# Kernel optimization log

Measured on AMD Instinct MI355X. Metric: run time of the kernel, lower is better.

## Reference

```python
import jax, jax.numpy as jnp
import numpy as np

RCUT = 6.0
NA = 10000      # atoms per image
NS = 4          # species
NMAX = 32       # radial basis size
NO = 4          # orbitals for lmax=2: (3**2-1)//2
OIDX = jnp.array([0, 1, 1, 1])  # lmax=2 -> [0] + [1]*3
B, NM = 4, 150000


def setup_inputs() -> dict:
    key = jax.random.key(0)
    ks = jax.random.split(key, 12)
    disp = jax.random.normal(ks[0], (B, NM, 3), jnp.float32) * 2.0
    iidx = jnp.sort(jax.random.randint(ks[1], (B, NM), 0, NA), axis=-1)
    jidx = jax.random.randint(ks[2], (B, NM), 0, NA)
    sorted_numbers = jax.random.randint(ks[3], (NA,), 0, NS)
    alpha = -(jax.random.uniform(ks[4], (NS, NMAX), jnp.float32) + 0.2)
    rs = jax.random.uniform(ks[5], (NS, NMAX), jnp.float32)
    species_params = jax.random.uniform(ks[6], (NS, NMAX), jnp.float32)
    # loop x lmax x nmax x NO
    orbital_params = jax.random.uniform(ks[7], (2, 2, NMAX, NO), jnp.float32)
    h1, h2 = int(1.2 * NO), int(1.2 * NMAX)  # 4, 38
    w1 = jax.random.normal(ks[8], (NO, h1), jnp.float32) * 0.3
    b1 = jnp.zeros((h1,), jnp.float32)
    w2 = jax.random.normal(ks[9], (h1, h2), jnp.float32) * 0.3
    b2 = jnp.zeros((h2,), jnp.float32)
    w3 = jax.random.normal(ks[10], (h2, NMAX), jnp.float32) * 0.3
    b3 = jnp.zeros((NMAX,), jnp.float32)
    return dict(disp=disp, alpha=alpha, rs=rs, species_params=species_params,
                orbital_params=orbital_params, w1=w1, b1=b1, w2=w2, b2=b2,
                w3=w3, b3=b3, iidx=iidx, jidx=jidx,
                sorted_numbers=sorted_numbers)


def _density(Wln, Csn, Fxyz, iidx, jidx):
    # Wln: NO x nmax x NO ; Csn: NA x nmax ; Fxyz: NM x NO x nmax
    cj = Csn[jidx]                                   # NM x nmax (gather)
    cjF = cj[:, None, :] * Fxyz                      # NM x NO x nmax
    bnl = jax.ops.segment_sum(cjF, iidx, num_segments=NA)  # NA x NO x nmax (scatter-add)
    t = jnp.einsum('lno,aln->alo', Wln, bnl)         # NA x NO x NO
    return jnp.sum(t * t, axis=1)                    # NA x NO


def _mlp(rho, w1, b1, w2, b2, w3, b3):
    h = jnp.tanh(rho @ w1 + b1)
    h = jnp.tanh(h @ w2 + b2)
    return h @ w3 + b3                               # NA x nmax


def reference(disp, alpha, rs, species_params, orbital_params,
              w1, b1, w2, b2, w3, b3, iidx, jidx, sorted_numbers):
    def one_image(disp_i, ii, jj):
        dist = jnp.linalg.norm(disp_i, axis=1)                        # NM
        fcut = 0.25 * (jnp.cos(dist * jnp.pi / RCUT) + 1.0) ** 2      # NM
        jatn = sorted_numbers[jj]                                     # NM
        radial = jnp.exp(alpha[jatn] * (dist[:, None] - rs[jatn]) ** 2)  # NM x nmax
        angle = jnp.ones((disp_i.shape[0], NO), disp_i.dtype).at[:, 1:4].set(disp_i)
        Fxyz = fcut[:, None, None] * angle[:, :, None] * radial[:, None, :]  # NM x NO x nmax
        Csn = species_params[sorted_numbers]                          # NA x nmax
        rho = _density(orbital_params[0][OIDX], Csn, Fxyz, ii, jj)    # NA x NO
        # loop iteration 1 (loop=2): shared per-atom MLP update of Csn
        Csn = Csn + _mlp(rho, w1, b1, w2, b2, w3, b3)
        rho = _density(orbital_params[1][OIDX], Csn, Fxyz, ii, jj)
        return rho
    return jax.vmap(one_image)(disp, iidx, jidx)                      # B x NA x NO
```

## Files before the change

kernel.cpp:

```cpp
#include <hip/hip_runtime.h>
#include <hip/hip_fp16.h>
#include <math.h>

#define NA_ 10000
#define NM_ 150000
#define B_  4
#define NS_ 4
#define NMAX_ 32
#define NO_ 4
#define H1_ 4
#define H2_ 38
#define PI_F 3.14159265358979323846f
#define LOG2E_F 1.44269504088896f

#define CSN_OFF   ((size_t)0)
#define CSN_BYTES ((size_t)B_ * NA_ * NMAX_ * 4)
#define ST_OFF    (CSN_OFF + CSN_BYTES)
#define ST_BYTES  ((size_t)B_ * (NA_ + 1) * 4 + 64)
#define E_OFF     (ST_OFF + ST_BYTES)
#define E_BYTES   (((size_t)B_ * NM_ + 64) * NMAX_ * 2)
#define WS_NEED_E (E_OFF + E_BYTES)

__device__ __forceinline__ float fast_tanh(float x) {
    float t = __expf(2.0f * x);
    return 1.0f - __fdividef(2.0f, t + 1.0f);
}

template <int CTRL>
__device__ __forceinline__ float dpp_ror_add(float v) {
    int r = __builtin_amdgcn_update_dpp(0, __float_as_int(v), CTRL, 0xF, 0xF, true);
    return v + __int_as_float(r);
}
__device__ __forceinline__ float half_reduce32(float v) {
    v = dpp_ror_add<0x121>(v);
    v = dpp_ror_add<0x122>(v);
    v = dpp_ror_add<0x124>(v);
    v = dpp_ror_add<0x128>(v);
    int s = __builtin_amdgcn_ds_swizzle(__float_as_int(v), 0x401F);
    return v + __int_as_float(s);
}

__global__ void starts_kernel(const int* __restrict__ iidx, int* __restrict__ starts) {
    int p = blockIdx.x * blockDim.x + threadIdx.x;
    if (p >= B_ * NM_) return;
    int b = p / NM_, pl = p - b * NM_;
    const int* ii = iidx + (size_t)b * NM_;
    int* st = starts + (size_t)b * (NA_ + 1);
    int cur = ii[pl];
    int prev = (pl == 0) ? -1 : ii[pl - 1];
    for (int a = prev + 1; a <= cur; ++a) st[a] = pl;
    if (pl == NM_ - 1) {
        for (int a = cur + 1; a <= NA_; ++a) st[a] = NM_;
    }
}

__global__ __launch_bounds__(256, 8) void pass0_kernel(
    const float* __restrict__ disp, const int* __restrict__ jidx,
    const float* __restrict__ alpha, const float* __restrict__ rsp,
    const float* __restrict__ spp, const float* __restrict__ op,
    const float* __restrict__ w1, const float* __restrict__ b1,
    const float* __restrict__ w2, const float* __restrict__ b2,
    const float* __restrict__ w3, const float* __restrict__ b3,
    const int* __restrict__ sorted_numbers, const int* __restrict__ starts,
    float* __restrict__ csn2, unsigned short* __restrict__ E)
{
    __shared__ float4 lds_rec[4][2][32];
    __shared__ float2 lds_df[4][2][32];
    __shared__ float2 tab2[NS_ * NMAX_];
    __shared__ float lds_h2[4][2][40];

    int tid = threadIdx.x;
    if (tid < NS_ * NMAX_)
        tab2[tid] = make_float2(alpha[tid] * LOG2E_F, rsp[tid]);
    __syncthreads();

    int wv = tid >> 6;
    int wave = blockIdx.x * 4 + wv;
    int lane = tid & 63;
    int h = lane >> 5, n = lane & 31;
    int g = wave * 2 + h;
    if (g >= B_ * NA_) return;
    int b = g / NA_, a = g - b * NA_;

    const int* st = starts + b * (NA_ + 1);
    int p0 = st[a], p1 = st[a + 1];
    int seg = p1 - p0;
    int oseg = __shfl_xor(seg, 32);
    int mseg = (seg > oseg) ? seg : oseg;

    const int* jjb = jidx + (size_t)b * NM_;
    const float* dpb = disp + (size_t)b * NM_ * 3;

    int pk = p0 + n;
    if (pk > NM_ - 1) pk = NM_ - 1;
    int jmine = jjb[pk];
    float sx = dpb[pk * 3 + 0];
    float sy = dpb[pk * 3 + 1];
    float sz = dpb[pk * 3 + 2];
    int jatm = sorted_numbers[jmine];
    float sd = sqrtf(sx * sx + sy * sy + sz * sz);
    float sc = __cosf(sd * (PI_F / 6.0f));
    float sfc = 0.25f * (sc + 1.f) * (sc + 1.f);
    lds_rec[wv][h][n] = make_float4(sx, sy, sz, __int_as_float(jatm));
    lds_df[wv][h][n] = make_float2(sd, sfc);
    const float4* lp = &lds_rec[wv][h][0];
    const float4* ldf4 = reinterpret_cast<const float4*>(&lds_df[wv][h][0]);
    const float2* tab2n = tab2 + n;

    float sp0 = spp[n], sp1 = spp[32 + n], sp2 = spp[64 + n], sp3 = spp[96 + n];

    float W0[NO_], W1[NO_];
#pragma unroll
    for (int o = 0; o < NO_; ++o) {
        W0[o] = op[(0 * NMAX_ + n) * NO_ + o];
        W1[o] = op[(1 * NMAX_ + n) * NO_ + o];
    }

    unsigned short* Ebl = E + ((size_t)b * NM_ + p0) * NMAX_ + n;

    float acc0 = 0.f, acc1 = 0.f, acc2 = 0.f, acc3 = 0.f;

#define KKF(k, DD, FF) {                                                     \
    float4 q_ = lp[(k)];                                                     \
    int jat_ = __float_as_int(q_.w);                                         \
    float2 ar_ = tab2n[jat_ * NMAX_];                                        \
    float dd_ = (DD) - ar_.y;                                                \
    float e_ = exp2f(ar_.x * dd_ * dd_);                                     \
    float Ef_ = e_ * (FF);                                                   \
    Ebl[(k) * NMAX_] = __half_as_ushort(__float2half_rn(Ef_));               \
    bool s0_ = (jat_ & 1) != 0;                                              \
    bool s1_ = (jat_ & 2) != 0;                                              \
    float cv_ = s1_ ? (s0_ ? sp3 : sp2) : (s0_ ? sp1 : sp0);                 \
    float coef_ = Ef_ * cv_;                                                 \
    coef_ = ((k) < seg) ? coef_ : 0.f;                                       \
    acc0 += coef_;                                                           \
    acc1 = fmaf(coef_, q_.x, acc1);                                          \
    acc2 = fmaf(coef_, q_.y, acc2);                                          \
    acc3 = fmaf(coef_, q_.z, acc3);                                          \
}
#define KK4F(k0) if (mseg > (k0)) {                                          \
    float4 dA_ = ldf4[(k0) >> 1];                                            \
    float4 dB_ = ldf4[((k0) >> 1) + 1];                                      \
    KKF(k0, dA_.x, dA_.y) KKF((k0)+1, dA_.z, dA_.w)                          \
    KKF((k0)+2, dB_.x, dB_.y) KKF((k0)+3, dB_.z, dB_.w) }
    KK4F(0) KK4F(4) KK4F(8) KK4F(12) KK4F(16) KK4F(20) KK4F(24) KK4F(28)
#undef KK4F
#undef KKF

    for (int p = p0 + 32; p < p1; ++p) {
        int j = jjb[p];
        float x = dpb[p * 3 + 0], y = dpb[p * 3 + 1], z = dpb[p * 3 + 2];
        int jat = sorted_numbers[j];
        float dist = sqrtf(x * x + y * y + z * z);
        float c = __cosf(dist * (PI_F / 6.0f));
        float fc = 0.25f * (c + 1.f) * (c + 1.f);
        float2 ar = tab2n[(jat & 3) * NMAX_];
        float dd = dist - ar.y;
        float Ef = fc * exp2f(ar.x * dd * dd);
        E[((size_t)b * NM_ + p) * NMAX_ + n] =
            __half_as_ushort(__float2half_rn(Ef));
        bool s0 = (jat & 1) != 0, s1 = (jat & 2) != 0;
        float cv = s1 ? (s0 ? sp3 : sp2) : (s0 ? sp1 : sp0);
        float coef = Ef * cv;
        acc0 += coef;
        acc1 = fmaf(coef, x, acc1);
        acc2 = fmaf(coef, y, acc2);
        acc3 = fmaf(coef, z, acc3);
    }

    float t[4][NO_];
#pragma unroll
    for (int o = 0; o < NO_; ++o) {
        t[0][o] = W0[o] * acc0;
        t[1][o] = W1[o] * acc1;
        t[2][o] = W1[o] * acc2;
        t[3][o] = W1[o] * acc3;
    }
#pragma unroll
    for (int l = 0; l < 4; ++l)
#pragma unroll
        for (int o = 0; o < NO_; ++o)
            t[l][o] = half_reduce32(t[l][o]);

    float rho[NO_];
#pragma unroll
    for (int o = 0; o < NO_; ++o)
        rho[o] = t[0][o] * t[0][o] + t[1][o] * t[1][o] +
                 t[2][o] * t[2][o] + t[3][o] * t[3][o];

    float h1v[H1_];
#pragma unroll
    for (int k = 0; k < H1_; ++k) {
        float s = b1[k];
#pragma unroll
        for (int o = 0; o < NO_; ++o) s = fmaf(rho[o], w1[o * H1_ + k], s);
        h1v[k] = fast_tanh(s);
    }
    float sa = b2[n];
    int jbi = 32 + (n < 6 ? n : 5);
    float sb = b2[jbi];
#pragma unroll
    for (int k = 0; k < H1_; ++k) {
        sa = fmaf(h1v[k], w2[k * H2_ + n], sa);
        sb = fmaf(h1v[k], w2[k * H2_ + jbi], sb);
    }
    float hva = fast_tanh(sa);
    float hvb = fast_tanh(sb);
    lds_h2[wv][h][n] = hva;
    if (n < 6) lds_h2[wv][h][32 + n] = hvb;
    const float4* h4 = reinterpret_cast<const float4*>(&lds_h2[wv][h][0]);
    float on = b3[n];
#pragma unroll
    for (int q = 0; q < 9; ++q) {
        float4 hh = h4[q];
        on = fmaf(hh.x, w3[(q * 4 + 0) * NMAX_ + n], on);
        on = fmaf(hh.y, w3[(q * 4 + 1) * NMAX_ + n], on);
        on = fmaf(hh.z, w3[(q * 4 + 2) * NMAX_ + n], on);
        on = fmaf(hh.w, w3[(q * 4 + 3) * NMAX_ + n], on);
    }
    float2 ht = *reinterpret_cast<const float2*>(&lds_h2[wv][h][36]);
    on = fmaf(ht.x, w3[36 * NMAX_ + n], on);
    on = fmaf(ht.y, w3[37 * NMAX_ + n], on);

    int aat = sorted_numbers[a];
    bool t0b = (aat & 1) != 0, t1b = (aat & 2) != 0;
    float basev = t1b ? (t0b ? sp3 : sp2) : (t0b ? sp1 : sp0);
    csn2[(size_t)g * NMAX_ + n] = basev + on;
}

__global__ __launch_bounds__(256, 4) void pass1_kernel(
    const float* __restrict__ disp, const int* __restrict__ jidx,
    const float* __restrict__ op, const int* __restrict__ starts,
    const float* __restrict__ csn2, const unsigned short* __restrict__ E,
    float* __restrict__ out)
{
    __shared__ float4 lds_rec[4][2][32];
    int tid = threadIdx.x;
    int wv = tid >> 6;
    int wave = blockIdx.x * 4 + wv;
    int lane = tid & 63;
    int h = lane >> 5, n = lane & 31;
    int g = wave * 2 + h;
    if (g >= B_ * NA_) return;
    int b = g / NA_, a = g - b * NA_;

    const int* st = starts + b * (NA_ + 1);
    int p0 = st[a], p1 = st[a + 1];
    int seg = p1 - p0;
    int oseg = __shfl_xor(seg, 32);
    int mseg = (seg > oseg) ? seg : oseg;

    const int* jjb = jidx + (size_t)b * NM_;
    const float* dpb = disp + (size_t)b * NM_ * 3;
    const float* csb = csn2 + (size_t)b * NA_ * NMAX_;

    int pk = p0 + n;
    if (pk > NM_ - 1) pk = NM_ - 1;
    int jmine = jjb[pk];
    float sx = dpb[pk * 3 + 0];
    float sy = dpb[pk * 3 + 1];
    float sz = dpb[pk * 3 + 2];
    lds_rec[wv][h][n] = make_float4(sx, sy, sz, __int_as_float(jmine));
    const float4* lp = &lds_rec[wv][h][0];
    const int* lpi = (const int*)lp;

    float W0[NO_], W1[NO_];
#pragma unroll
    for (int o = 0; o < NO_; ++o) {
        W0[o] = op[(2 * NMAX_ + n) * NO_ + o];
        W1[o] = op[(3 * NMAX_ + n) * NO_ + o];
    }

    const unsigned short* Erd = E + ((size_t)b * NM_ + p0) * NMAX_ + n;

    float cj[32];
    unsigned short r[32];
#define LC(k) { int j_ = lpi[(k) * 4 + 3];                                   \
                cj[(k)] = csb[(size_t)j_ * NMAX_ + n]; }
#define LC8(k0) LC(k0) LC((k0)+1) LC((k0)+2) LC((k0)+3) \
                LC((k0)+4) LC((k0)+5) LC((k0)+6) LC((k0)+7)
    LC8(0)
    if (mseg > 8)  { LC8(8) }  else { cj[8]=cj[9]=cj[10]=cj[11]=cj[12]=cj[13]=cj[14]=cj[15]=0.f; }
    if (mseg > 16) { LC8(16) } else { cj[16]=cj[17]=cj[18]=cj[19]=cj[20]=cj[21]=cj[22]=cj[23]=0.f; }
    if (mseg > 24) { LC8(24) } else { cj[24]=cj[25]=cj[26]=cj[27]=cj[28]=cj[29]=cj[30]=cj[31]=0.f; }
#undef LC8
#undef LC
#define LDR(k) r[(k)] = Erd[(k) * NMAX_];
#define LDR8(k0) LDR(k0) LDR((k0)+1) LDR((k0)+2) LDR((k0)+3) \
                 LDR((k0)+4) LDR((k0)+5) LDR((k0)+6) LDR((k0)+7)
    LDR8(0)
    if (mseg > 8)  { LDR8(8) }  else { r[8]=r[9]=r[10]=r[11]=r[12]=r[13]=r[14]=r[15]=0; }
    if (mseg > 16) { LDR8(16) } else { r[16]=r[17]=r[18]=r[19]=r[20]=r[21]=r[22]=r[23]=0; }
    if (mseg > 24) { LDR8(24) } else { r[24]=r[25]=r[26]=r[27]=r[28]=r[29]=r[30]=r[31]=0; }
#undef LDR8
#undef LDR

    float acc0 = 0.f, acc1 = 0.f, acc2 = 0.f, acc3 = 0.f;
#define KK(k) {                                                              \
    float4 q_ = lp[(k)];                                                     \
    float coef_ = __half2float(__ushort_as_half(r[(k)])) * cj[(k)];          \
    coef_ = ((k) < seg) ? coef_ : 0.f;                                       \
    acc0 += coef_;                                                           \
    acc1 = fmaf(coef_, q_.x, acc1);                                          \
    acc2 = fmaf(coef_, q_.y, acc2);                                          \
    acc3 = fmaf(coef_, q_.z, acc3);                                          \
}
#define KK4(k0) if (mseg > (k0)) { KK(k0) KK((k0)+1) KK((k0)+2) KK((k0)+3) }
    KK4(0) KK4(4) KK4(8) KK4(12) KK4(16) KK4(20) KK4(24) KK4(28)
#undef KK4
#undef KK

    for (int p = p0 + 32; p < p1; ++p) {
        int j = jjb[p];
        float x = dpb[p * 3 + 0], y = dpb[p * 3 + 1], z = dpb[p * 3 + 2];
        float Ef = __half2float(__ushort_as_half(
            E[((size_t)b * NM_ + p) * NMAX_ + n]));
        float coef = Ef * csb[(size_t)j * NMAX_ + n];
        acc0 += coef;
        acc1 = fmaf(coef, x, acc1);
        acc2 = fmaf(coef, y, acc2);
        acc3 = fmaf(coef, z, acc3);
    }

    float t[4][NO_];
#pragma unroll
    for (int o = 0; o < NO_; ++o) {
        t[0][o] = W0[o] * acc0;
        t[1][o] = W1[o] * acc1;
        t[2][o] = W1[o] * acc2;
        t[3][o] = W1[o] * acc3;
    }
#pragma unroll
    for (int l = 0; l < 4; ++l)
#pragma unroll
        for (int o = 0; o < NO_; ++o)
            t[l][o] = half_reduce32(t[l][o]);

    float rho[NO_];
#pragma unroll
    for (int o = 0; o < NO_; ++o)
        rho[o] = t[0][o] * t[0][o] + t[1][o] * t[1][o] +
                 t[2][o] * t[2][o] + t[3][o] * t[3][o];

    if (n == 0) {
        *reinterpret_cast<float4*>(out + (size_t)g * NO_) =
            make_float4(rho[0], rho[1], rho[2], rho[3]);
    }
}

template <int PASS>
__global__ __launch_bounds__(256, 4) void fb_pass_kernel(
    const float* __restrict__ disp, const int* __restrict__ jidx,
    const float* __restrict__ alpha, const float* __restrict__ rsp,
    const float* __restrict__ spp, const float* __restrict__ op,
    const float* __restrict__ w1, const float* __restrict__ b1,
    const float* __restrict__ w2, const float* __restrict__ b2,
    const float* __restrict__ w3, const float* __restrict__ b3,
    const int* __restrict__ sorted_numbers, const int* __restrict__ starts,
    float* __restrict__ csn2, float* __restrict__ out)
{
    __shared__ float4 lds_rec[4][2][32];
    __shared__ float2 lds_df[4][2][32];
    __shared__ float2 tab2[NS_ * NMAX_];
    __shared__ float lds_h2[4][2][40];

    int tid = threadIdx.x;
    if (tid < NS_ * NMAX_)
        tab2[tid] = make_float2(alpha[tid] * LOG2E_F, rsp[tid]);
    __syncthreads();

    int wv = tid >> 6;
    int wave = blockIdx.x * 4 + wv;
    int lane = tid & 63;
    int h = lane >> 5, n = lane & 31;
    int g = wave * 2 + h;
    if (g >= B_ * NA_) return;
    int b = g / NA_, a = g - b * NA_;

    const int* st = starts + b * (NA_ + 1);
    int p0 = st[a], p1 = st[a + 1];
    int seg = p1 - p0;
    int oseg = __shfl_xor(seg, 32);
    int mseg = (seg > oseg) ? seg : oseg;

    const int* jjb = jidx + (size_t)b * NM_;
    const float* dpb = disp + (size_t)b * NM_ * 3;
    const float* csb = csn2 + (size_t)b * NA_ * NMAX_;

    int pk = p0 + n;
    if (pk > NM_ - 1) pk = NM_ - 1;
    int jmine = jjb[pk];
    float sx = dpb[pk * 3 + 0];
    float sy = dpb[pk * 3 + 1];
    float sz = dpb[pk * 3 + 2];
    int jatm = sorted_numbers[jmine];
    float sd = sqrtf(sx * sx + sy * sy + sz * sz);
    float sc = __cosf(sd * (PI_F / 6.0f));
    float sfc = 0.25f * (sc + 1.f) * (sc + 1.f);
    lds_rec[wv][h][n] = make_float4(sx, sy, sz,
                                    __int_as_float(jmine | (jatm << 14)));
    lds_df[wv][h][n] = make_float2(sd, sfc);
    const float4* lp = &lds_rec[wv][h][0];
    const int* lpi = (const int*)lp;
    const float4* ldf4 = reinterpret_cast<const float4*>(&lds_df[wv][h][0]);
    const float2* tab2n = tab2 + n;

    float sp0 = spp[n], sp1 = spp[32 + n], sp2 = spp[64 + n], sp3 = spp[96 + n];

    const float* opb = op + (size_t)PASS * 2 * NMAX_ * NO_;
    float W0[NO_], W1[NO_];
#pragma unroll
    for (int o = 0; o < NO_; ++o) {
        W0[o] = opb[(0 * NMAX_ + n) * NO_ + o];
        W1[o] = opb[(1 * NMAX_ + n) * NO_ + o];
    }

    float cj[32];
    if constexpr (PASS == 1) {
#define LC(k) { int w_ = lpi[(k) * 4 + 3] & 0x3fff;                          \
                cj[(k)] = csb[(size_t)w_ * NMAX_ + n]; }
#define LC8(k0) LC(k0) LC((k0)+1) LC((k0)+2) LC((k0)+3) \
                LC((k0)+4) LC((k0)+5) LC((k0)+6) LC((k0)+7)
        LC8(0)
        if (mseg > 8)  { LC8(8) }  else { cj[8]=cj[9]=cj[10]=cj[11]=cj[12]=cj[13]=cj[14]=cj[15]=0.f; }
        if (mseg > 16) { LC8(16) } else { cj[16]=cj[17]=cj[18]=cj[19]=cj[20]=cj[21]=cj[22]=cj[23]=0.f; }
        if (mseg > 24) { LC8(24) } else { cj[24]=cj[25]=cj[26]=cj[27]=cj[28]=cj[29]=cj[30]=cj[31]=0.f; }
#undef LC8
#undef LC
    }

    float acc0 = 0.f, acc1 = 0.f, acc2 = 0.f, acc3 = 0.f;
#define KKF(k, DD, FF) {                                                     \
    float4 q_ = lp[(k)];                                                     \
    int w_ = __float_as_int(q_.w);                                           \
    int jat_ = (w_ >> 14) & 3;                                               \
    float2 ar_ = tab2n[jat_ * NMAX_];                                        \
    float dd_ = (DD) - ar_.y;                                                \
    float e_ = exp2f(ar_.x * dd_ * dd_);                                     \
    float Ef_ = e_ * (FF);                                                   \
    float cv_;                                                               \
    if constexpr (PASS == 0) {                                               \
        bool s0_ = (w_ & (1 << 14)) != 0;                                    \
        bool s1_ = (w_ & (1 << 15)) != 0;                                    \
        cv_ = s1_ ? (s0_ ? sp3 : sp2) : (s0_ ? sp1 : sp0);                   \
    } else {                                                                 \
        cv_ = cj[(k)];                                                       \
    }                                                                        \
    float coef_ = Ef_ * cv_;                                                 \
    coef_ = ((k) < seg) ? coef_ : 0.f;                                       \
    acc0 += coef_;                                                           \
    acc1 = fmaf(coef_, q_.x, acc1);                                          \
    acc2 = fmaf(coef_, q_.y, acc2);                                          \
    acc3 = fmaf(coef_, q_.z, acc3);                                          \
}
#define KK4F(k0) if (mseg > (k0)) {                                          \
    float4 dA_ = ldf4[(k0) >> 1];                                            \
    float4 dB_ = ldf4[((k0) >> 1) + 1];                                      \
    KKF(k0, dA_.x, dA_.y) KKF((k0)+1, dA_.z, dA_.w)                          \
    KKF((k0)+2, dB_.x, dB_.y) KKF((k0)+3, dB_.z, dB_.w) }
    KK4F(0) KK4F(4) KK4F(8) KK4F(12) KK4F(16) KK4F(20) KK4F(24) KK4F(28)
#undef KK4F
#undef KKF

    for (int p = p0 + 32; p < p1; ++p) {
        int j = jjb[p];
        float x = dpb[p * 3 + 0], y = dpb[p * 3 + 1], z = dpb[p * 3 + 2];
        int jat = sorted_numbers[j];
        float dist = sqrtf(x * x + y * y + z * z);
        float c = __cosf(dist * (PI_F / 6.0f));
        float fc = 0.25f * (c + 1.f) * (c + 1.f);
        float2 ar = tab2n[(jat & 3) * NMAX_];
        float dd = dist - ar.y;
        float Ef = fc * exp2f(ar.x * dd * dd);
        float cv;
        if constexpr (PASS == 0) {
            bool s0 = (jat & 1) != 0, s1 = (jat & 2) != 0;
            cv = s1 ? (s0 ? sp3 : sp2) : (s0 ? sp1 : sp0);
        } else {
            cv = csb[(size_t)j * NMAX_ + n];
        }
        float coef = Ef * cv;
        acc0 += coef;
        acc1 = fmaf(coef, x, acc1);
        acc2 = fmaf(coef, y, acc2);
        acc3 = fmaf(coef, z, acc3);
    }

    float t[4][NO_];
#pragma unroll
    for (int o = 0; o < NO_; ++o) {
        t[0][o] = W0[o] * acc0;
        t[1][o] = W1[o] * acc1;
        t[2][o] = W1[o] * acc2;
        t[3][o] = W1[o] * acc3;
    }
#pragma unroll
    for (int l = 0; l < 4; ++l)
#pragma unroll
        for (int o = 0; o < NO_; ++o)
            t[l][o] = half_reduce32(t[l][o]);

    float rho[NO_];
#pragma unroll
    for (int o = 0; o < NO_; ++o)
        rho[o] = t[0][o] * t[0][o] + t[1][o] * t[1][o] +
                 t[2][o] * t[2][o] + t[3][o] * t[3][o];

    if constexpr (PASS == 1) {
        if (n == 0) {
            *reinterpret_cast<float4*>(out + (size_t)g * NO_) =
                make_float4(rho[0], rho[1], rho[2], rho[3]);
        }
    } else {
        float h1v[H1_];
#pragma unroll
        for (int k = 0; k < H1_; ++k) {
            float s = b1[k];
#pragma unroll
            for (int o = 0; o < NO_; ++o) s = fmaf(rho[o], w1[o * H1_ + k], s);
            h1v[k] = fast_tanh(s);
        }
        float sa = b2[n];
        int jbi = 32 + (n < 6 ? n : 5);
        float sb = b2[jbi];
#pragma unroll
        for (int k = 0; k < H1_; ++k) {
            sa = fmaf(h1v[k], w2[k * H2_ + n], sa);
            sb = fmaf(h1v[k], w2[k * H2_ + jbi], sb);
        }
        float hva = fast_tanh(sa);
        float hvb = fast_tanh(sb);
        lds_h2[wv][h][n] = hva;
        if (n < 6) lds_h2[wv][h][32 + n] = hvb;
        const float4* h4 = reinterpret_cast<const float4*>(&lds_h2[wv][h][0]);
        float on = b3[n];
#pragma unroll
        for (int q = 0; q < 9; ++q) {
            float4 hh = h4[q];
            on = fmaf(hh.x, w3[(q * 4 + 0) * NMAX_ + n], on);
            on = fmaf(hh.y, w3[(q * 4 + 1) * NMAX_ + n], on);
            on = fmaf(hh.z, w3[(q * 4 + 2) * NMAX_ + n], on);
            on = fmaf(hh.w, w3[(q * 4 + 3) * NMAX_ + n], on);
        }
        float2 ht = *reinterpret_cast<const float2*>(&lds_h2[wv][h][36]);
        on = fmaf(ht.x, w3[36 * NMAX_ + n], on);
        on = fmaf(ht.y, w3[37 * NMAX_ + n], on);

        int aat = sorted_numbers[a];
        bool t0b = (aat & 1) != 0, t1b = (aat & 2) != 0;
        float basev = t1b ? (t0b ? sp3 : sp2) : (t0b ? sp1 : sp0);
        csn2[(size_t)g * NMAX_ + n] = basev + on;
    }
}

extern "C" void kernel_launch(void* const* d_in, const int* in_sizes, int n_in,
                              void* d_out, int out_size, void* d_ws, size_t ws_size,
                              hipStream_t stream) {
    const float* disp = (const float*)d_in[0];
    const float* alpha = (const float*)d_in[1];
    const float* rsp = (const float*)d_in[2];
    const float* spp = (const float*)d_in[3];
    const float* op = (const float*)d_in[4];
    const float* w1 = (const float*)d_in[5];
    const float* b1 = (const float*)d_in[6];
    const float* w2 = (const float*)d_in[7];
    const float* b2 = (const float*)d_in[8];
    const float* w3 = (const float*)d_in[9];
    const float* b3 = (const float*)d_in[10];
    const int* iidx = (const int*)d_in[11];
    const int* jidx = (const int*)d_in[12];
    const int* sn = (const int*)d_in[13];
    float* out = (float*)d_out;

    float* csn2 = (float*)((char*)d_ws + CSN_OFF);
    int* starts = (int*)((char*)d_ws + ST_OFF);
    unsigned short* E = (unsigned short*)((char*)d_ws + E_OFF);

    int nthr = B_ * NM_;
    starts_kernel<<<(nthr + 255) / 256, 256, 0, stream>>>(iidx, starts);

    int ablocks = (B_ * NA_) / 8;
    if (ws_size >= WS_NEED_E) {
        pass0_kernel<<<ablocks, 256, 0, stream>>>(disp, jidx, alpha, rsp, spp,
                                                  op, w1, b1, w2, b2, w3, b3,
                                                  sn, starts, csn2, E);
        pass1_kernel<<<ablocks, 256, 0, stream>>>(disp, jidx, op, starts,
                                                  csn2, E, out);
    } else {
        fb_pass_kernel<0><<<ablocks, 256, 0, stream>>>(disp, jidx, alpha, rsp,
                                                       spp, op, w1, b1, w2, b2,
                                                       w3, b3, sn, starts,
                                                       csn2, out);
        fb_pass_kernel<1><<<ablocks, 256, 0, stream>>>(disp, jidx, alpha, rsp,
                                                       spp, op, w1, b1, w2, b2,
                                                       w3, b3, sn, starts,
                                                       csn2, out);
    }
}
```

Before: 64.84 us.

## Split radial table computation into pair-parallel prep kernel before atom pass

Moves computation of the fp16 radial*cutoff table E out of the per-atom pass0 kernel into a separate pair-parallel kernel, so the work is spread evenly over all pairs instead of over atoms with uneven segment lengths. The atom pass then reads E back and only does the accumulation and MLP. Alpha/rs lookups now use per-lane register selects with __expf instead of an LDS table, and the MLP hidden layer is broadcast with cross-lane shuffles instead of LDS. The cost is an extra kernel launch and an extra read of E from memory.

```diff
diff --git a/kernel.cpp b/kernel.cpp
--- a/kernel.cpp
+++ b/kernel.cpp
@@ -11,7 +11,6 @@
 #define H1_ 4
 #define H2_ 38
 #define PI_F 3.14159265358979323846f
-#define LOG2E_F 1.44269504088896f
 
 #define CSN_OFF   ((size_t)0)
 #define CSN_BYTES ((size_t)B_ * NA_ * NMAX_ * 4)
@@ -54,26 +53,49 @@
     }
 }
 
-__global__ __launch_bounds__(256, 8) void pass0_kernel(
+__global__ __launch_bounds__(256, 8) void prep0_kernel(
     const float* __restrict__ disp, const int* __restrict__ jidx,
     const float* __restrict__ alpha, const float* __restrict__ rsp,
+    const int* __restrict__ sorted_numbers, unsigned short* __restrict__ E)
+{
+    int tid = threadIdx.x;
+    int lane = tid & 63;
+    int h = lane >> 5, n = lane & 31;
+    int gp = blockIdx.x * 8 + (tid >> 6) * 2 + h;
+    if (gp >= B_ * NM_) return;
+
+    float al0 = alpha[n],      al1 = alpha[32 + n];
+    float al2 = alpha[64 + n], al3 = alpha[96 + n];
+    float rv0 = rsp[n],        rv1 = rsp[32 + n];
+    float rv2 = rsp[64 + n],   rv3 = rsp[96 + n];
+
+    int j = jidx[gp];
+    int b = gp / NM_;
+    int jat = sorted_numbers[(size_t)b * NA_ * 0 + j];
+    const float* dp = disp + (size_t)gp * 3;
+    float x = dp[0], y = dp[1], z = dp[2];
+    float dist = sqrtf(x * x + y * y + z * z);
+    float c = __cosf(dist * (PI_F / 6.0f));
+    float fc = 0.25f * (c + 1.f) * (c + 1.f);
+    bool s0 = (jat & 1) != 0, s1 = (jat & 2) != 0;
+    float av = s1 ? (s0 ? al3 : al2) : (s0 ? al1 : al0);
+    float rv = s1 ? (s0 ? rv3 : rv2) : (s0 ? rv1 : rv0);
+    float dd = dist - rv;
+    float Ef = fc * __expf(av * dd * dd);
+    E[(size_t)gp * NMAX_ + n] = __half_as_ushort(__float2half_rn(Ef));
+}
+
+__global__ __launch_bounds__(256, 4) void pass0_light_kernel(
+    const float* __restrict__ disp, const int* __restrict__ jidx,
     const float* __restrict__ spp, const float* __restrict__ op,
     const float* __restrict__ w1, const float* __restrict__ b1,
     const float* __restrict__ w2, const float* __restrict__ b2,
     const float* __restrict__ w3, const float* __restrict__ b3,
     const int* __restrict__ sorted_numbers, const int* __restrict__ starts,
-    float* __restrict__ csn2, unsigned short* __restrict__ E)
+    const unsigned short* __restrict__ E, float* __restrict__ csn2)
 {
     __shared__ float4 lds_rec[4][2][32];
-    __shared__ float2 lds_df[4][2][32];
-    __shared__ float2 tab2[NS_ * NMAX_];
-    __shared__ float lds_h2[4][2][40];
-
     int tid = threadIdx.x;
-    if (tid < NS_ * NMAX_)
-        tab2[tid] = make_float2(alpha[tid] * LOG2E_F, rsp[tid]);
-    __syncthreads();
-
     int wv = tid >> 6;
     int wave = blockIdx.x * 4 + wv;
     int lane = tid & 63;
@@ -94,18 +116,12 @@
     int pk = p0 + n;
     if (pk > NM_ - 1) pk = NM_ - 1;
     int jmine = jjb[pk];
+    int jatm = sorted_numbers[jmine];
     float sx = dpb[pk * 3 + 0];
     float sy = dpb[pk * 3 + 1];
     float sz = dpb[pk * 3 + 2];
-    int jatm = sorted_numbers[jmine];
-    float sd = sqrtf(sx * sx + sy * sy + sz * sz);
-    float sc = __cosf(sd * (PI_F / 6.0f));
-    float sfc = 0.25f * (sc + 1.f) * (sc + 1.f);
     lds_rec[wv][h][n] = make_float4(sx, sy, sz, __int_as_float(jatm));
-    lds_df[wv][h][n] = make_float2(sd, sfc);
     const float4* lp = &lds_rec[wv][h][0];
-    const float4* ldf4 = reinterpret_cast<const float4*>(&lds_df[wv][h][0]);
-    const float2* tab2n = tab2 + n;
 
     float sp0 = spp[n], sp1 = spp[32 + n], sp2 = spp[64 + n], sp3 = spp[96 + n];
 
@@ -116,49 +132,43 @@
         W1[o] = op[(1 * NMAX_ + n) * NO_ + o];
     }
 
-    unsigned short* Ebl = E + ((size_t)b * NM_ + p0) * NMAX_ + n;
+    const unsigned short* Erd = E + ((size_t)b * NM_ + p0) * NMAX_ + n;
+    unsigned short r[32];
+#define LDR(k) r[(k)] = Erd[(k) * NMAX_];
+#define LDR8(k0) LDR(k0) LDR((k0)+1) LDR((k0)+2) LDR((k0)+3) \
+                 LDR((k0)+4) LDR((k0)+5) LDR((k0)+6) LDR((k0)+7)
+    LDR8(0)
+    if (mseg > 8)  { LDR8(8) }  else { r[8]=r[9]=r[10]=r[11]=r[12]=r[13]=r[14]=r[15]=0; }
+    if (mseg > 16) { LDR8(16) } else { r[16]=r[17]=r[18]=r[19]=r[20]=r[21]=r[22]=r[23]=0; }
+    if (mseg > 24) { LDR8(24) } else { r[24]=r[25]=r[26]=r[27]=r[28]=r[29]=r[30]=r[31]=0; }
+#undef LDR8
+#undef LDR
 
     float acc0 = 0.f, acc1 = 0.f, acc2 = 0.f, acc3 = 0.f;
-
-#define KKF(k, DD, FF) {                                                     \
+#define KK(k) {                                                              \
     float4 q_ = lp[(k)];                                                     \
     int jat_ = __float_as_int(q_.w);                                         \
-    float2 ar_ = tab2n[jat_ * NMAX_];                                        \
-    float dd_ = (DD) - ar_.y;                                                \
-    float e_ = exp2f(ar_.x * dd_ * dd_);                                     \
-    float Ef_ = e_ * (FF);                                                   \
-    Ebl[(k) * NMAX_] = __half_as_ushort(__float2half_rn(Ef_));               \
     bool s0_ = (jat_ & 1) != 0;                                              \
     bool s1_ = (jat_ & 2) != 0;                                              \
     float cv_ = s1_ ? (s0_ ? sp3 : sp2) : (s0_ ? sp1 : sp0);                 \
-    float coef_ = Ef_ * cv_;                                                 \
+    float coef_ = __half2float(__ushort_as_half(r[(k)])) * cv_;              \
     coef_ = ((k) < seg) ? coef_ : 0.f;                                       \
     acc0 += coef_;                                                           \
     acc1 = fmaf(coef_, q_.x, acc1);                                          \
     acc2 = fmaf(coef_, q_.y, acc2);                                          \
     acc3 = fmaf(coef_, q_.z, acc3);                                          \
 }
-#define KK4F(k0) if (mseg > (k0)) {                                          \
-    float4 dA_ = ldf4[(k0) >> 1];                                            \
-    float4 dB_ = ldf4[((k0) >> 1) + 1];                                      \
-    KKF(k0, dA_.x, dA_.y) KKF((k0)+1, dA_.z, dA_.w)                          \
-    KKF((k0)+2, dB_.x, dB_.y) KKF((k0)+3, dB_.z, dB_.w) }
-    KK4F(0) KK4F(4) KK4F(8) KK4F(12) KK4F(16) KK4F(20) KK4F(24) KK4F(28)
-#undef KK4F
-#undef KKF
+#define KK4(k0) if (mseg > (k0)) { KK(k0) KK((k0)+1) KK((k0)+2) KK((k0)+3) }
+    KK4(0) KK4(4) KK4(8) KK4(12) KK4(16) KK4(20) KK4(24) KK4(28)
+#undef KK4
+#undef KK
 
     for (int p = p0 + 32; p < p1; ++p) {
         int j = jjb[p];
         float x = dpb[p * 3 + 0], y = dpb[p * 3 + 1], z = dpb[p * 3 + 2];
         int jat = sorted_numbers[j];
-        float dist = sqrtf(x * x + y * y + z * z);
-        float c = __cosf(dist * (PI_F / 6.0f));
-        float fc = 0.25f * (c + 1.f) * (c + 1.f);
-        float2 ar = tab2n[(jat & 3) * NMAX_];
-        float dd = dist - ar.y;
-        float Ef = fc * exp2f(ar.x * dd * dd);
-        E[((size_t)b * NM_ + p) * NMAX_ + n] =
-            __half_as_ushort(__float2half_rn(Ef));
+        float Ef = __half2float(__ushort_as_half(
+            E[((size_t)b * NM_ + p) * NMAX_ + n]));
         bool s0 = (jat & 1) != 0, s1 = (jat & 2) != 0;
         float cv = s1 ? (s0 ? sp3 : sp2) : (s0 ? sp1 : sp0);
         float coef = Ef * cv;
@@ -188,6 +198,8 @@
         rho[o] = t[0][o] * t[0][o] + t[1][o] * t[1][o] +
                  t[2][o] * t[2][o] + t[3][o] * t[3][o];
 
+    int hb = lane & 32;
+
     float h1v[H1_];
 #pragma unroll
     for (int k = 0; k < H1_; ++k) {
@@ -206,22 +218,17 @@
     }
     float hva = fast_tanh(sa);
     float hvb = fast_tanh(sb);
-    lds_h2[wv][h][n] = hva;
-    if (n < 6) lds_h2[wv][h][32 + n] = hvb;
-    const float4* h4 = reinterpret_cast<const float4*>(&lds_h2[wv][h][0]);
     float on = b3[n];
 #pragma unroll
-    for (int q = 0; q < 9; ++q) {
-        float4 hh = h4[q];
-        on = fmaf(hh.x, w3[(q * 4 + 0) * NMAX_ + n], on);
-        on = fmaf(hh.y, w3[(q * 4 + 1) * NMAX_ + n], on);
-        on = fmaf(hh.z, w3[(q * 4 + 2) * NMAX_ + n], on);
-        on = fmaf(hh.w, w3[(q * 4 + 3) * NMAX_ + n], on);
-    }
-    float2 ht = *reinterpret_cast<const float2*>(&lds_h2[wv][h][36]);
-    on = fmaf(ht.x, w3[36 * NMAX_ + n], on);
-    on = fmaf(ht.y, w3[37 * NMAX_ + n], on);
-
+    for (int j2 = 0; j2 < 32; ++j2) {
+        float hj = __shfl(hva, hb + j2);
+        on = fmaf(hj, w3[j2 * NMAX_ + n], on);
+    }
+#pragma unroll
+    for (int j2 = 0; j2 < 6; ++j2) {
+        float hj = __shfl(hvb, hb + j2);
+        on = fmaf(hj, w3[(32 + j2) * NMAX_ + n], on);
+    }
     int aat = sorted_numbers[a];
     bool t0b = (aat & 1) != 0, t1b = (aat & 2) != 0;
     float basev = t1b ? (t0b ? sp3 : sp2) : (t0b ? sp1 : sp0);
@@ -361,14 +368,7 @@
 {
     __shared__ float4 lds_rec[4][2][32];
     __shared__ float2 lds_df[4][2][32];
-    __shared__ float2 tab2[NS_ * NMAX_];
-    __shared__ float lds_h2[4][2][40];
-
     int tid = threadIdx.x;
-    if (tid < NS_ * NMAX_)
-        tab2[tid] = make_float2(alpha[tid] * LOG2E_F, rsp[tid]);
-    __syncthreads();
-
     int wv = tid >> 6;
     int wave = blockIdx.x * 4 + wv;
     int lane = tid & 63;
@@ -403,8 +403,11 @@
     const float4* lp = &lds_rec[wv][h][0];
     const int* lpi = (const int*)lp;
     const float4* ldf4 = reinterpret_cast<const float4*>(&lds_df[wv][h][0]);
-    const float2* tab2n = tab2 + n;
-
+
+    float al0 = alpha[n],      al1 = alpha[32 + n];
+    float al2 = alpha[64 + n], al3 = alpha[96 + n];
+    float rv0 = rsp[n],        rv1 = rsp[32 + n];
+    float rv2 = rsp[64 + n],   rv3 = rsp[96 + n];
     float sp0 = spp[n], sp1 = spp[32 + n], sp2 = spp[64 + n], sp3 = spp[96 + n];
 
     const float* opb = op + (size_t)PASS * 2 * NMAX_ * NO_;
@@ -433,15 +436,15 @@
 #define KKF(k, DD, FF) {                                                     \
     float4 q_ = lp[(k)];                                                     \
     int w_ = __float_as_int(q_.w);                                           \
-    int jat_ = (w_ >> 14) & 3;                                               \
-    float2 ar_ = tab2n[jat_ * NMAX_];                                        \
-    float dd_ = (DD) - ar_.y;                                                \
-    float e_ = exp2f(ar_.x * dd_ * dd_);                                     \
+    bool s0_ = (w_ & (1 << 14)) != 0;                                        \
+    bool s1_ = (w_ & (1 << 15)) != 0;                                        \
+    float av_ = s1_ ? (s0_ ? al3 : al2) : (s0_ ? al1 : al0);                 \
+    float rv_ = s1_ ? (s0_ ? rv3 : rv2) : (s0_ ? rv1 : rv0);                 \
+    float dd_ = (DD) - rv_;                                                  \
+    float e_ = __expf(av_ * dd_ * dd_);                                      \
     float Ef_ = e_ * (FF);                                                   \
     float cv_;                                                               \
     if constexpr (PASS == 0) {                                               \
-        bool s0_ = (w_ & (1 << 14)) != 0;                                    \
-        bool s1_ = (w_ & (1 << 15)) != 0;                                    \
         cv_ = s1_ ? (s0_ ? sp3 : sp2) : (s0_ ? sp1 : sp0);                   \
     } else {                                                                 \
         cv_ = cj[(k)];                                                       \
@@ -469,16 +472,16 @@
         float dist = sqrtf(x * x + y * y + z * z);
         float c = __cosf(dist * (PI_F / 6.0f));
         float fc = 0.25f * (c + 1.f) * (c + 1.f);
-        float2 ar = tab2n[(jat & 3) * NMAX_];
-        float dd = dist - ar.y;
-        float Ef = fc * exp2f(ar.x * dd * dd);
+        bool s0 = (jat & 1) != 0, s1 = (jat & 2) != 0;
+        float av = s1 ? (s0 ? al3 : al2) : (s0 ? al1 : al0);
+        float rv = s1 ? (s0 ? rv3 : rv2) : (s0 ? rv1 : rv0);
+        float dd = dist - rv;
+        float Ef = fc * __expf(av * dd * dd);
         float cv;
-        if constexpr (PASS == 0) {
-            bool s0 = (jat & 1) != 0, s1 = (jat & 2) != 0;
+        if constexpr (PASS == 0)
             cv = s1 ? (s0 ? sp3 : sp2) : (s0 ? sp1 : sp0);
-        } else {
+        else
             cv = csb[(size_t)j * NMAX_ + n];
-        }
         float coef = Ef * cv;
         acc0 += coef;
         acc1 = fmaf(coef, x, acc1);
@@ -505,6 +508,8 @@
     for (int o = 0; o < NO_; ++o)
         rho[o] = t[0][o] * t[0][o] + t[1][o] * t[1][o] +
                  t[2][o] * t[2][o] + t[3][o] * t[3][o];
+
+    int hb = lane & 32;
 
     if constexpr (PASS == 1) {
         if (n == 0) {
@@ -530,22 +535,17 @@
         }
         float hva = fast_tanh(sa);
         float hvb = fast_tanh(sb);
-        lds_h2[wv][h][n] = hva;
-        if (n < 6) lds_h2[wv][h][32 + n] = hvb;
-        const float4* h4 = reinterpret_cast<const float4*>(&lds_h2[wv][h][0]);
         float on = b3[n];
 #pragma unroll
-        for (int q = 0; q < 9; ++q) {
-            float4 hh = h4[q];
-            on = fmaf(hh.x, w3[(q * 4 + 0) * NMAX_ + n], on);
-            on = fmaf(hh.y, w3[(q * 4 + 1) * NMAX_ + n], on);
-            on = fmaf(hh.z, w3[(q * 4 + 2) * NMAX_ + n], on);
-            on = fmaf(hh.w, w3[(q * 4 + 3) * NMAX_ + n], on);
+        for (int j2 = 0; j2 < 32; ++j2) {
+            float hj = __shfl(hva, hb + j2);
+            on = fmaf(hj, w3[j2 * NMAX_ + n], on);
         }
-        float2 ht = *reinterpret_cast<const float2*>(&lds_h2[wv][h][36]);
-        on = fmaf(ht.x, w3[36 * NMAX_ + n], on);
-        on = fmaf(ht.y, w3[37 * NMAX_ + n], on);
-
+#pragma unroll
+        for (int j2 = 0; j2 < 6; ++j2) {
+            float hj = __shfl(hvb, hb + j2);
+            on = fmaf(hj, w3[(32 + j2) * NMAX_ + n], on);
+        }
         int aat = sorted_numbers[a];
         bool t0b = (aat & 1) != 0, t1b = (aat & 2) != 0;
         float basev = t1b ? (t0b ? sp3 : sp2) : (t0b ? sp1 : sp0);
@@ -581,9 +581,11 @@
 
     int ablocks = (B_ * NA_) / 8;
     if (ws_size >= WS_NEED_E) {
-        pass0_kernel<<<ablocks, 256, 0, stream>>>(disp, jidx, alpha, rsp, spp,
-                                                  op, w1, b1, w2, b2, w3, b3,
-                                                  sn, starts, csn2, E);
+        int pblocks = (B_ * NM_) / 8;
+        prep0_kernel<<<pblocks, 256, 0, stream>>>(disp, jidx, alpha, rsp, sn, E);
+        pass0_light_kernel<<<ablocks, 256, 0, stream>>>(disp, jidx, spp, op,
+                                                        w1, b1, w2, b2, w3, b3,
+                                                        sn, starts, E, csn2);
         pass1_kernel<<<ablocks, 256, 0, stream>>>(disp, jidx, op, starts,
                                                   csn2, E, out);
     } else {
```

Result: slower. 97.35 us (+50.1%).
